# Kernel optimization log

Hardware: AMD Instinct MI355X
Metric: run time of the kernel (lower is better)

Reference implementation:

```python
import jax, jax.numpy as jnp
from jax import lax
import numpy as np

B, N, D_IN = 8, 8192, 16
GROUP_NUM, K = 512, 32
OUT_DIM, N_BLOCKS, DIM_EXP = 256, 2, 2
PREV_DIM = OUT_DIM // DIM_EXP   # 128
MID = OUT_DIM // 2              # bottleneck width in FeatureTransform
C_EXP = 2 * PREV_DIM + 3        # linear1 input channels
EPS = 1e-5                      # BatchNorm eps (eval mode, running stats mean=0 var=1)


def setup_inputs() -> dict:
    ks = jax.random.split(jax.random.key(0), 8)
    return {
        "xyz": jax.random.normal(ks[0], (B, N, 3), jnp.float32),
        "feat": jax.random.normal(ks[1], (B, N, D_IN), jnp.float32),
        "w_embed": jax.random.normal(ks[2], (PREV_DIM, D_IN), jnp.float32) * 0.1,
        "b_embed": jnp.zeros((PREV_DIM,), jnp.float32),
        "g_embed": jnp.ones((PREV_DIM,), jnp.float32),
        "be_embed": jnp.zeros((PREV_DIM,), jnp.float32),
        "w_lin1": jax.random.normal(ks[3], (OUT_DIM, C_EXP), jnp.float32) * 0.05,
        "g_lin1": jnp.ones((OUT_DIM,), jnp.float32),
        "be_lin1": jnp.zeros((OUT_DIM,), jnp.float32),
        "down_w": jax.random.normal(ks[4], (N_BLOCKS, MID, OUT_DIM), jnp.float32) * 0.05,
        "down_b": jnp.zeros((N_BLOCKS, MID), jnp.float32),
        "gd": jnp.ones((N_BLOCKS, MID), jnp.float32),
        "bd": jnp.zeros((N_BLOCKS, MID), jnp.float32),
        "up_w": jax.random.normal(ks[5], (N_BLOCKS, OUT_DIM, MID), jnp.float32) * 0.05,
        "up_b": jnp.zeros((N_BLOCKS, OUT_DIM), jnp.float32),
        "gu": jnp.ones((N_BLOCKS, OUT_DIM), jnp.float32),
        "bu": jnp.zeros((N_BLOCKS, OUT_DIM), jnp.float32),
    }


def _bn(x, g, b, axis):
    # eval-mode BatchNorm with running mean=0, var=1
    shp = [1] * x.ndim
    shp[axis] = -1
    return x / jnp.sqrt(1.0 + EPS) * g.reshape(shp) + b.reshape(shp)


def _fps(xyz, n):
    # deterministic FPS (eval mode): start from point farthest from origin
    Bb, Nn, _ = xyz.shape
    cur0 = jnp.argmax(jnp.sum(xyz * xyz, -1), axis=1)          # [B]
    mind0 = jnp.full((Bb, Nn), 1e10, xyz.dtype)

    def step(carry, _):
        cur, mind = carry
        c = jnp.take_along_axis(xyz, cur[:, None, None], axis=1)  # [B,1,3]
        mind = jnp.minimum(mind, jnp.sum((xyz - c) ** 2, -1))
        return (jnp.argmax(mind, axis=1), mind), cur

    _, sel = lax.scan(step, (cur0, mind0), None, length=n)     # sel: [n,B]
    return sel.T                                               # [B,n]


def _gather(points, idx):
    # points [B,N,C], idx [B,...] -> [B,...,C]
    Bb = points.shape[0]
    flat = idx.reshape(Bb, -1)
    out = jnp.take_along_axis(points, flat[:, :, None], axis=1)
    return out.reshape(idx.shape + (points.shape[-1],))


def _knn(k, ref, query):
    # squared dists, clamped at 0 as in pairwise_sq_dist
    d = (jnp.sum(query * query, -1)[:, :, None]
         + jnp.sum(ref * ref, -1)[:, None, :]
         - 2.0 * jnp.einsum('bsc,bnc->bsn', query, ref))
    d = jnp.maximum(d, 0.0)
    _, idx = lax.top_k(-d, k)
    return idx  # [B,S,k]


def reference(xyz, feat, w_embed, b_embed, g_embed, be_embed, w_lin1, g_lin1, be_lin1,
              down_w, down_b, gd, bd, up_w, up_b, gu, bu):
    # PointEmbed: conv1d(1x1) + BN + ReLU on per-point features -> [B,N,PREV_DIM]
    f0 = jnp.einsum('bnc,dc->bnd', feat, w_embed) + b_embed
    f0 = jax.nn.relu(_bn(f0, g_embed, be_embed, axis=2))

    # FpsKnnGroup
    sel = _fps(xyz, GROUP_NUM)                  # [B,G]
    lc_xyz = _gather(xyz, sel)                  # [B,G,3]
    lc_feat = _gather(f0, sel)                  # [B,G,PREV_DIM]
    nn_idx = _knn(K, xyz, lc_xyz)               # [B,G,K]
    knn_xyz = _gather(xyz, nn_idx)              # [B,G,K,3]
    knn_feat = jnp.concatenate([_gather(f0, nn_idx), knn_xyz], axis=-1)  # [B,G,K,PREV+3]

    # LocalGeoAgg, norm_type='mn40'
    anchor = lc_xyz[:, :, None, :]
    rel_raw = knn_xyz - anchor
    std = jnp.std(rel_raw, ddof=1) + 1e-5       # torch .std() is unbiased
    knn_xyz_n = rel_raw / std
    Bc = knn_feat.shape[0]
    expanded = jnp.concatenate(
        [knn_feat, jnp.broadcast_to(lc_feat[:, :, None, :], (Bc, GROUP_NUM, K, PREV_DIM))],
        axis=-1)                                # [B,G,K,C_EXP]
    x = jnp.einsum('bgkc,dc->bdgk', expanded, w_lin1)   # linear1 (no bias)
    x = jax.nn.relu(_bn(x, g_lin1, be_lin1, axis=1))    # [B,OUT_DIM,G,K]

    # GaussianPosEnc: rel = normalized knn_xyz (perm) minus raw lc_xyz center
    rel = knn_xyz_n.transpose(0, 3, 1, 2) - lc_xyz.transpose(0, 2, 1)[:, :, :, None]
    w = jnp.exp(-jnp.linalg.norm(rel, axis=1) / 2.0)    # sigma=1 -> 2*sigma^2=2
    x = x * w[:, None, :, :]

    # FeatureTransform residual bottlenecks
    for i in range(N_BLOCKS):
        h = jnp.einsum('bcgk,mc->bmgk', x, down_w[i]) + down_b[i][None, :, None, None]
        h = jax.nn.relu(_bn(h, gd[i], bd[i], axis=1))
        h = jnp.einsum('bcgk,mc->bmgk', h, up_w[i]) + up_b[i][None, :, None, None]
        h = _bn(h, gu[i], bu[i], axis=1)
        x = jax.nn.relu(h + x)

    # MaxMeanPool over K
    return jnp.max(x, axis=-1) + jnp.mean(x, axis=-1)   # [B,OUT_DIM,G]
```

## Files before the change

### kernel.cpp

```cpp
#include <hip/hip_runtime.h>

#define B_ 8
#define N_ 8192
#define DIN_ 16
#define G_ 512
#define K_ 32
#define OD_ 256
#define PD_ 128
#define MD_ 128
#define CE_ 259
#define EST 168
#define XST2 264
#define HST 136
#define AL1K 160

typedef __attribute__((ext_vector_type(8))) short short8t;
typedef __attribute__((ext_vector_type(4))) float f32x4;
#define MFMA16(a, b, c) __builtin_amdgcn_mfma_f32_16x16x32_bf16((a), (b), (c), 0, 0, 0)

__device__ __forceinline__ ushort bf16_rne(float x) {
    unsigned u = __float_as_uint(x);
    return (ushort)((u + 0x7FFFu + ((u >> 16) & 1u)) >> 16);
}
__device__ __forceinline__ void bf16_split(float x, ushort& h, ushort& l) {
    h = bf16_rne(x);
    float hf = __uint_as_float((unsigned)h << 16);
    l = bf16_rne(x - hf);
}

#define DPP_STEP_MAXF(x, ctrl) { int _t = __builtin_amdgcn_update_dpp(            \
        __float_as_int(x), __float_as_int(x), (ctrl), 0xF, 0xF, false);           \
        (x) = fmaxf((x), __int_as_float(_t)); }
#define DPP_STEP_MINF(x, ctrl) { int _t = __builtin_amdgcn_update_dpp(            \
        __float_as_int(x), __float_as_int(x), (ctrl), 0xF, 0xF, false);           \
        (x) = fminf((x), __int_as_float(_t)); }
#define DPP_STEP_MINU(x, ctrl) { int _t = __builtin_amdgcn_update_dpp(            \
        (int)(x), (int)(x), (ctrl), 0xF, 0xF, false);                             \
        unsigned _u = (unsigned)_t; (x) = ((x) < _u) ? (x) : _u; }

__device__ __forceinline__ float wave_max_f32(float x) {
    DPP_STEP_MAXF(x, 0x121); DPP_STEP_MAXF(x, 0x122);
    DPP_STEP_MAXF(x, 0x124); DPP_STEP_MAXF(x, 0x128);
    DPP_STEP_MAXF(x, 0x142); DPP_STEP_MAXF(x, 0x143);
    return __int_as_float(__builtin_amdgcn_readlane(__float_as_int(x), 63));
}
__device__ __forceinline__ float wave_min_f32(float x) {
    DPP_STEP_MINF(x, 0x121); DPP_STEP_MINF(x, 0x122);
    DPP_STEP_MINF(x, 0x124); DPP_STEP_MINF(x, 0x128);
    DPP_STEP_MINF(x, 0x142); DPP_STEP_MINF(x, 0x143);
    return __int_as_float(__builtin_amdgcn_readlane(__float_as_int(x), 63));
}
__device__ __forceinline__ unsigned wave_min_u32(unsigned x) {
    DPP_STEP_MINU(x, 0x121); DPP_STEP_MINU(x, 0x122);
    DPP_STEP_MINU(x, 0x124); DPP_STEP_MINU(x, 0x128);
    DPP_STEP_MINU(x, 0x142); DPP_STEP_MINU(x, 0x143);
    return (unsigned)__builtin_amdgcn_readlane((int)x, 63);
}

__global__ __launch_bounds__(256)
void prep_kernel(const float* __restrict__ w_lin1, const float* __restrict__ down_w,
                 const float* __restrict__ up_w, const float* __restrict__ w_embed,
                 float* __restrict__ wta, float* __restrict__ wEtg,
                 ushort* __restrict__ alf, ushort* __restrict__ adf,
                 ushort* __restrict__ auf) {
    int i = blockIdx.x * blockDim.x + threadIdx.x;
    if (i < PD_ * OD_) {
        int j = i >> 8, c = i & 255;
        wta[i] = w_lin1[c * CE_ + 131 + j];
    }
    if (i < DIN_ * PD_) {
        int r = i >> 7, c = i & 127;
        wEtg[i] = w_embed[c * DIN_ + r];
    }
    if (i < 5120) {
        int lane = i & 63, t = i >> 6;
        int kbi = t % 5, mtile = t / 5;
        int m = mtile * 16 + (lane & 15), g16 = lane >> 4;
        int dst = i * 8;
#pragma unroll
        for (int j = 0; j < 8; ++j) {
            int k = kbi * 32 + g16 * 8 + j;
            float v = (k < 131) ? w_lin1[m * CE_ + k] : 0.f;
            ushort h, l; bf16_split(v, h, l);
            alf[dst + j] = h; alf[dst + j + 40960] = l;
        }
    }
    if (i < 8192) {
        int lane = i & 63, t = i >> 6;
        int kbi = t & 7, mtile = (t >> 3) & 7, l = t >> 6;
        int m = mtile * 16 + (lane & 15), g16 = lane >> 4;
        int dst = i * 8;
#pragma unroll
        for (int j = 0; j < 8; ++j) {
            int k = kbi * 32 + g16 * 8 + j;
            float v = down_w[(l * MD_ + m) * OD_ + k];
            ushort h, lo; bf16_split(v, h, lo);
            adf[dst + j] = h; adf[dst + j + 65536] = lo;
        }
    }
    if (i < 8192) {
        int lane = i & 63, t = i >> 6;
        int kbi = t & 3, mtile = (t >> 2) & 15, l = t >> 6;
        int m = mtile * 16 + (lane & 15), g16 = lane >> 4;
        int dst = i * 8;
#pragma unroll
        for (int j = 0; j < 8; ++j) {
            int k = kbi * 32 + g16 * 8 + j;
            float v = up_w[(l * OD_ + m) * MD_ + k];
            ushort h, lo; bf16_split(v, h, lo);
            auf[dst + j] = h; auf[dst + j + 65536] = lo;
        }
    }
}

__global__ __launch_bounds__(512)
void fps_kernel(const float* __restrict__ xyz, int* __restrict__ sel) {
#pragma clang fp contract(off)
    __shared__ float sx[N_], sy[N_], sz[N_];
    __shared__ unsigned long long wred[2][8];
    int b = blockIdx.x, tid = threadIdx.x;
    const float* xb = xyz + (size_t)b * N_ * 3;
    for (int i = tid; i < N_; i += 512) {
        sx[i] = xb[i * 3]; sy[i] = xb[i * 3 + 1]; sz[i] = xb[i * 3 + 2];
    }
    __syncthreads();
    float px[16], py[16], pz[16], mind[16];
#pragma unroll
    for (int j = 0; j < 16; ++j) {
        int idx = tid + j * 512;
        px[j] = sx[idx]; py[j] = sy[idx]; pz[j] = sz[idx];
        mind[j] = 1e10f;
    }
    float tv[16]; int tj[16];
#pragma unroll
    for (int j = 0; j < 16; ++j) {
        tv[j] = (px[j] * px[j] + py[j] * py[j]) + pz[j] * pz[j];
        tj[j] = j;
    }
#pragma unroll
    for (int s = 8; s > 0; s >>= 1)
#pragma unroll
        for (int p = 0; p < 16; p += 16 / s) {
        }
    float v8[8]; int j8[8];
#pragma unroll
    for (int p = 0; p < 8; ++p) { bool t = tv[2*p+1] > tv[2*p]; v8[p] = t ? tv[2*p+1] : tv[2*p]; j8[p] = t ? tj[2*p+1] : tj[2*p]; }
    float v4[4]; int j4[4];
#pragma unroll
    for (int p = 0; p < 4; ++p) { bool t = v8[2*p+1] > v8[2*p]; v4[p] = t ? v8[2*p+1] : v8[2*p]; j4[p] = t ? j8[2*p+1] : j8[2*p]; }
    float v2[2]; int j2[2];
#pragma unroll
    for (int p = 0; p < 2; ++p) { bool t = v4[2*p+1] > v4[2*p]; v2[p] = t ? v4[2*p+1] : v4[2*p]; j2[p] = t ? j4[2*p+1] : j4[2*p]; }
    bool t0 = v2[1] > v2[0];
    float bv = t0 ? v2[1] : v2[0];
    int bi = tid + (t0 ? j2[1] : j2[0]) * 512;

    int wv = tid >> 6;
    {
        float wm = wave_max_f32(bv);
        unsigned mi = (bv == wm) ? (unsigned)bi : 0xFFFFFFFFu;
        unsigned wi = wave_min_u32(mi);
        if ((tid & 63) == 0)
            wred[0][wv] = ((unsigned long long)__float_as_uint(wm) << 32)
                        | (unsigned long long)(0xFFFFFFFFu - wi);
    }
    __syncthreads();
    unsigned long long best = wred[0][0];
#pragma unroll
    for (int i = 1; i < 8; ++i) { unsigned long long v = wred[0][i]; if (v > best) best = v; }
    int cur = (int)(0xFFFFFFFFu - (unsigned)(best & 0xFFFFFFFFull));

    for (int it = 0; it < G_; ++it) {
        if (tid == 0) sel[b * G_ + it] = cur;
        float cx = sx[cur], cy = sy[cur], cz = sz[cur];
#pragma unroll
        for (int j = 0; j < 16; ++j) {
            float dx = px[j] - cx, dy = py[j] - cy, dz = pz[j] - cz;
            float d = (dx * dx + dy * dy) + dz * dz;
            float m = fminf(mind[j], d); mind[j] = m;
        }
#pragma unroll
        for (int p = 0; p < 8; ++p) { bool t = mind[2*p+1] > mind[2*p]; v8[p] = t ? mind[2*p+1] : mind[2*p]; j8[p] = t ? (2*p+1) : (2*p); }
#pragma unroll
        for (int p = 0; p < 4; ++p) { bool t = v8[2*p+1] > v8[2*p]; v4[p] = t ? v8[2*p+1] : v8[2*p]; j4[p] = t ? j8[2*p+1] : j8[2*p]; }
#pragma unroll
        for (int p = 0; p < 2; ++p) { bool t = v4[2*p+1] > v4[2*p]; v2[p] = t ? v4[2*p+1] : v4[2*p]; j2[p] = t ? j4[2*p+1] : j4[2*p]; }
        t0 = v2[1] > v2[0];
        bv = t0 ? v2[1] : v2[0];
        bi = tid + (t0 ? j2[1] : j2[0]) * 512;

        float wm = wave_max_f32(bv);
        unsigned mi = (bv == wm) ? (unsigned)bi : 0xFFFFFFFFu;
        unsigned wi = wave_min_u32(mi);
        int pb = (it + 1) & 1;
        if ((tid & 63) == 0)
            wred[pb][wv] = ((unsigned long long)__float_as_uint(wm) << 32)
                         | (unsigned long long)(0xFFFFFFFFu - wi);
        __syncthreads();
        best = wred[pb][0];
#pragma unroll
        for (int i = 1; i < 8; ++i) { unsigned long long v = wred[pb][i]; if (v > best) best = v; }
        cur = (int)(0xFFFFFFFFu - (unsigned)(best & 0xFFFFFFFFull));
    }
}

__global__ __launch_bounds__(256)
void knn_kernel(const float* __restrict__ xyz, const int* __restrict__ sel,
                int* __restrict__ nn) {
#pragma clang fp contract(off)
    __shared__ float dld[N_];
    __shared__ unsigned long long wred[2][4];
    int gb = blockIdx.x; int b = gb >> 9, s = gb & (G_ - 1);
    const float* xb = xyz + (size_t)b * N_ * 3;
    int q = sel[b * G_ + s];
    float qx = xb[q * 3], qy = xb[q * 3 + 1], qz = xb[q * 3 + 2];
    float qq = (qx * qx + qy * qy) + qz * qz;
    int tid = threadIdx.x;
    const float FINF = __builtin_inff();
    float lv = FINF; int li = tid;
#pragma unroll 4
    for (int j = 0; j < 32; ++j) {
        int n = tid + j * 256;
        float rx = xb[n * 3], ry = xb[n * 3 + 1], rz = xb[n * 3 + 2];
        float rr = (rx * rx + ry * ry) + rz * rz;
        float dt = (qx * rx + qy * ry) + qz * rz;
        float d = (qq + rr) - 2.0f * dt;
        d = fmaxf(d, 0.f);
        dld[n] = d;
        if (d < lv) { lv = d; li = n; }
    }
    {
        float wm = wave_min_f32(lv);
        unsigned mi = (lv == wm) ? (unsigned)li : 0xFFFFFFFFu;
        unsigned wi = wave_min_u32(mi);
        if ((tid & 63) == 0)
            wred[0][tid >> 6] = ((unsigned long long)__float_as_uint(wm) << 32)
                              | (unsigned long long)wi;
    }
    __syncthreads();
    unsigned long long best = wred[0][0];
#pragma unroll
    for (int i = 1; i < 4; ++i) { unsigned long long v = wred[0][i]; if (v < best) best = v; }
    int win = (int)(best & 0xFFFFFFFFull);

    for (int t = 0; t < K_; ++t) {
        if (tid == 0) nn[(size_t)gb * K_ + t] = win;
        if ((win & 255) == tid) {
            dld[win] = FINF;
            lv = FINF; li = tid;
            for (int j = 0; j < 32; ++j) {
                float d = dld[tid + j * 256];
                if (d < lv) { lv = d; li = tid + j * 256; }
            }
        }
        float wm = wave_min_f32(lv);
        unsigned mi = (lv == wm) ? (unsigned)li : 0xFFFFFFFFu;
        unsigned wi = wave_min_u32(mi);
        int pb = (t + 1) & 1;
        if ((tid & 63) == 0)
            wred[pb][tid >> 6] = ((unsigned long long)__float_as_uint(wm) << 32)
                               | (unsigned long long)wi;
        __syncthreads();
        best = wred[pb][0];
#pragma unroll
        for (int i = 1; i < 4; ++i) { unsigned long long v = wred[pb][i]; if (v < best) best = v; }
        win = (int)(best & 0xFFFFFFFFull);
    }
}

__global__ void std_acc_kernel(const float* __restrict__ xyz, const int* __restrict__ sel,
                               const int* __restrict__ nn, double* __restrict__ acc) {
    int tot = B_ * G_ * K_;
    int stride = gridDim.x * blockDim.x;
    double ls = 0.0, lss = 0.0;
    for (int idx = blockIdx.x * blockDim.x + threadIdx.x; idx < tot; idx += stride) {
        int b = idx >> 14; int g = (idx >> 5) & (G_ - 1);
        int n = nn[idx]; int a = sel[b * G_ + g];
        const float* xb = xyz + (size_t)b * N_ * 3;
#pragma unroll
        for (int c = 0; c < 3; ++c) {
            float v = xb[n * 3 + c] - xb[a * 3 + c];
            ls += (double)v; lss += (double)v * (double)v;
        }
    }
#pragma unroll
    for (int off = 32; off > 0; off >>= 1) {
        ls += __shfl_down(ls, off); lss += __shfl_down(lss, off);
    }
    if ((threadIdx.x & 63) == 0) { atomicAdd(acc, ls); atomicAdd(acc + 1, lss); }
}

__global__ void std_fin_kernel(const double* __restrict__ acc, float* __restrict__ stdp) {
    double s = acc[0], ss = acc[1];
    double M = (double)(B_ * G_ * K_ * 3);
    double var = (ss - s * s / M) / (M - 1.0);
    stdp[0] = (float)sqrt(var) + 1e-5f;
}

__global__ __launch_bounds__(256, 3)
void group_kernel(const float* __restrict__ xyz, const float* __restrict__ feat,
                  const float* __restrict__ wEtg, const float* __restrict__ bE,
                  const float* __restrict__ gE, const float* __restrict__ beE,
                  const int* __restrict__ sel, const int* __restrict__ nn,
                  const float* __restrict__ wta,
                  const ushort* __restrict__ alf, const ushort* __restrict__ adf,
                  const ushort* __restrict__ auf,
                  const float* __restrict__ g_lin1, const float* __restrict__ be_lin1,
                  const float* __restrict__ down_b, const float* __restrict__ gd,
                  const float* __restrict__ bd,
                  const float* __restrict__ up_b, const float* __restrict__ gu,
                  const float* __restrict__ bu,
                  const float* __restrict__ stdp, float* __restrict__ out) {
    __shared__ __align__(16) ushort smem[25600];
    __shared__ float lcv_s[OD_];
    __shared__ float wk_s[K_];
    __shared__ int nns_s[K_];
    __shared__ float anch[3];
    ushort* XTh = smem;
    ushort* XTl = smem + 8448;
    ushort* HTh = smem + 16896;
    ushort* HTl = smem + 21248;
    ushort* Ehi = XTh;
    ushort* Elo = XTl;
    float* wEt = (float*)(smem + 16896);
    float* fL  = wEt + 2048;
    float* lcf = fL + 544;

    int gb = blockIdx.x; int b = gb >> 9, g = gb & (G_ - 1);
    int tid = threadIdx.x;
    const float* xb = xyz + (size_t)b * N_ * 3;
    int a = sel[b * G_ + g];
    if (tid < K_) nns_s[tid] = nn[(size_t)gb * K_ + tid];
    if (tid < 3)  anch[tid] = xb[a * 3 + tid];
    __syncthreads();

    for (int idx = tid; idx < DIN_ * PD_; idx += 256) wEt[idx] = wEtg[idx];
    const float* fb = feat + (size_t)b * N_ * DIN_;
    for (int idx = tid; idx < 33 * DIN_; idx += 256) {
        int k = idx >> 4, j = idx & 15;
        int n = (k < K_) ? nns_s[k] : a;
        fL[idx] = fb[(size_t)n * DIN_ + j];
    }
    __syncthreads();

    const float s_bn = 1.0f / sqrtf(1.0f + 1e-5f);
    for (int idx = tid; idx < 33 * PD_; idx += 256) {
        int k = idx >> 7, c = idx & 127;
        const float* f = &fL[k * DIN_];
        float acc2 = 0.f;
#pragma unroll
        for (int i = 0; i < DIN_; ++i) acc2 += wEt[i * PD_ + c] * f[i];
        acc2 = (acc2 + bE[c]) * s_bn * gE[c] + beE[c];
        acc2 = fmaxf(acc2, 0.f);
        if (k < K_) { ushort h, l; bf16_split(acc2, h, l); Ehi[k * EST + c] = h; Elo[k * EST + c] = l; }
        else lcf[c] = acc2;
    }
    for (int idx = tid; idx < K_ * 32; idx += 256) {
        int k = idx >> 5, c = 128 + (idx & 31);
        ushort h = 0, l = 0;
        if (c < 131) { float v = xb[nns_s[k] * 3 + (c - 128)]; bf16_split(v, h, l); }
        Ehi[k * EST + c] = h; Elo[k * EST + c] = l;
    }
    if (tid < K_) {
#pragma clang fp contract(off)
        float sd = stdp[0];
        int n = nns_s[tid];
        float rx = (xb[n * 3]     - anch[0]) / sd - anch[0];
        float ry = (xb[n * 3 + 1] - anch[1]) / sd - anch[1];
        float rz = (xb[n * 3 + 2] - anch[2]) / sd - anch[2];
        float nrm = sqrtf((rx * rx + ry * ry) + rz * rz);
        wk_s[tid] = expf(-0.5f * nrm);
    }
    __syncthreads();
    {
        float s = 0.f;
        for (int j = 0; j < PD_; ++j) s += wta[j * OD_ + tid] * lcf[j];
        lcv_s[tid] = s;
    }
    __syncthreads();

    int wv = tid >> 6, lane = tid & 63;
    int g16 = lane >> 4, r16 = lane & 15;
    int lane8 = lane * 8;

    f32x4 accl[4][2];
#pragma unroll
    for (int mt = 0; mt < 4; ++mt) {
        int mc = 64 * wv + 16 * mt + 4 * g16;
        float4 lv = *(const float4*)&lcv_s[mc];
        f32x4 iv = {lv.x, lv.y, lv.z, lv.w};
        accl[mt][0] = iv; accl[mt][1] = iv;
    }
    {
        int eb0 = r16 * EST + g16 * 8;
        int eb1 = (r16 + 16) * EST + g16 * 8;
        for (int kbi = 0; kbi < 5; ++kbi) {
            int kb = kbi * 32;
            short8t eh0 = *(const short8t*)&Ehi[eb0 + kb];
            short8t el0 = *(const short8t*)&Elo[eb0 + kb];
            short8t eh1 = *(const short8t*)&Ehi[eb1 + kb];
            short8t el1 = *(const short8t*)&Elo[eb1 + kb];
#pragma unroll
            for (int mt = 0; mt < 4; ++mt) {
                const ushort* wp = alf + (((4 * wv + mt) * 5 + kbi) << 9) + lane8;
                short8t wh = *(const short8t*)wp;
                short8t wl = *(const short8t*)(wp + 40960);
                accl[mt][0] = MFMA16(wh, eh0, accl[mt][0]);
                accl[mt][1] = MFMA16(wh, eh1, accl[mt][1]);
                accl[mt][0] = MFMA16(wh, el0, accl[mt][0]);
                accl[mt][1] = MFMA16(wh, el1, accl[mt][1]);
                accl[mt][0] = MFMA16(wl, eh0, accl[mt][0]);
                accl[mt][1] = MFMA16(wl, eh1, accl[mt][1]);
            }
        }
    }
    __syncthreads();
    {
        float w0 = wk_s[r16], w1 = wk_s[r16 + 16];
#pragma unroll
        for (int mt = 0; mt < 4; ++mt) {
            int mc = 64 * wv + 16 * mt + 4 * g16;
            float4 gg = *(const float4*)&g_lin1[mc];
            float4 bb = *(const float4*)&be_lin1[mc];
            float ga[4] = {gg.x, gg.y, gg.z, gg.w};
            float ba[4] = {bb.x, bb.y, bb.z, bb.w};
            ushort h0[4], l0[4], h1[4], l1[4];
#pragma unroll
            for (int r = 0; r < 4; ++r) {
                float v0 = fmaxf(accl[mt][0][r] * s_bn * ga[r] + ba[r], 0.f) * w0;
                float v1 = fmaxf(accl[mt][1][r] * s_bn * ga[r] + ba[r], 0.f) * w1;
                bf16_split(v0, h0[r], l0[r]);
                bf16_split(v1, h1[r], l1[r]);
            }
            *(ushort4*)&XTh[r16 * XST2 + mc] = make_ushort4(h0[0], h0[1], h0[2], h0[3]);
            *(ushort4*)&XTl[r16 * XST2 + mc] = make_ushort4(l0[0], l0[1], l0[2], l0[3]);
            *(ushort4*)&XTh[(r16 + 16) * XST2 + mc] = make_ushort4(h1[0], h1[1], h1[2], h1[3]);
            *(ushort4*)&XTl[(r16 + 16) * XST2 + mc] = make_ushort4(l1[0], l1[1], l1[2], l1[3]);
        }
    }
    __syncthreads();

    int xbo0 = r16 * XST2 + g16 * 8;
    int xbo1 = (r16 + 16) * XST2 + g16 * 8;
    int hbo0 = r16 * HST + g16 * 8;
    int hbo1 = (r16 + 16) * HST + g16 * 8;
    const f32x4 zz = {0.f, 0.f, 0.f, 0.f};
    const float inv_k = 1.0f / 32.0f;

    for (int l = 0; l < 2; ++l) {
        f32x4 accd[2][2];
        accd[0][0] = zz; accd[0][1] = zz; accd[1][0] = zz; accd[1][1] = zz;
        for (int kbi = 0; kbi < 8; ++kbi) {
            int kb = kbi * 32;
            short8t xh0 = *(const short8t*)&XTh[xbo0 + kb];
            short8t xl0 = *(const short8t*)&XTl[xbo0 + kb];
            short8t xh1 = *(const short8t*)&XTh[xbo1 + kb];
            short8t xl1 = *(const short8t*)&XTl[xbo1 + kb];
#pragma unroll
            for (int mt = 0; mt < 2; ++mt) {
                const ushort* wp = adf + (((l * 8 + (2 * wv + mt)) * 8 + kbi) << 9) + lane8;
                short8t wh = *(const short8t*)wp;
                short8t wl = *(const short8t*)(wp + 65536);
                accd[mt][0] = MFMA16(wh, xh0, accd[mt][0]);
                accd[mt][1] = MFMA16(wh, xh1, accd[mt][1]);
                accd[mt][0] = MFMA16(wh, xl0, accd[mt][0]);
                accd[mt][1] = MFMA16(wh, xl1, accd[mt][1]);
                accd[mt][0] = MFMA16(wl, xh0, accd[mt][0]);
                accd[mt][1] = MFMA16(wl, xh1, accd[mt][1]);
            }
        }
#pragma unroll
        for (int mt = 0; mt < 2; ++mt) {
            int mc = 32 * wv + 16 * mt + 4 * g16;
            float4 db = *(const float4*)&down_b[l * MD_ + mc];
            float4 gv = *(const float4*)&gd[l * MD_ + mc];
            float4 bv = *(const float4*)&bd[l * MD_ + mc];
            float dba[4] = {db.x, db.y, db.z, db.w};
            float gva[4] = {gv.x, gv.y, gv.z, gv.w};
            float bva[4] = {bv.x, bv.y, bv.z, bv.w};
            ushort h0[4], l0[4], h1[4], l1[4];
#pragma unroll
            for (int r = 0; r < 4; ++r) {
                float v0 = fmaxf((accd[mt][0][r] + dba[r]) * s_bn * gva[r] + bva[r], 0.f);
                float v1 = fmaxf((accd[mt][1][r] + dba[r]) * s_bn * gva[r] + bva[r], 0.f);
                bf16_split(v0, h0[r], l0[r]);
                bf16_split(v1, h1[r], l1[r]);
            }
            *(ushort4*)&HTh[r16 * HST + mc] = make_ushort4(h0[0], h0[1], h0[2], h0[3]);
            *(ushort4*)&HTl[r16 * HST + mc] = make_ushort4(l0[0], l0[1], l0[2], l0[3]);
            *(ushort4*)&HTh[(r16 + 16) * HST + mc] = make_ushort4(h1[0], h1[1], h1[2], h1[3]);
            *(ushort4*)&HTl[(r16 + 16) * HST + mc] = make_ushort4(l1[0], l1[1], l1[2], l1[3]);
        }
        __syncthreads();

        f32x4 accu[4][2];
#pragma unroll
        for (int mt = 0; mt < 4; ++mt) { accu[mt][0] = zz; accu[mt][1] = zz; }
        for (int kbi = 0; kbi < 4; ++kbi) {
            int kb = kbi * 32;
            short8t hh0 = *(const short8t*)&HTh[hbo0 + kb];
            short8t hl0 = *(const short8t*)&HTl[hbo0 + kb];
            short8t hh1 = *(const short8t*)&HTh[hbo1 + kb];
            short8t hl1 = *(const short8t*)&HTl[hbo1 + kb];
#pragma unroll
            for (int mt = 0; mt < 4; ++mt) {
                const ushort* wp = auf + (((l * 16 + (4 * wv + mt)) * 4 + kbi) << 9) + lane8;
                short8t wh = *(const short8t*)wp;
                short8t wl = *(const short8t*)(wp + 65536);
                accu[mt][0] = MFMA16(wh, hh0, accu[mt][0]);
                accu[mt][1] = MFMA16(wh, hh1, accu[mt][1]);
                accu[mt][0] = MFMA16(wh, hl0, accu[mt][0]);
                accu[mt][1] = MFMA16(wh, hl1, accu[mt][1]);
                accu[mt][0] = MFMA16(wl, hh0, accu[mt][0]);
                accu[mt][1] = MFMA16(wl, hh1, accu[mt][1]);
            }
        }
#pragma unroll
        for (int mt = 0; mt < 4; ++mt) {
            int mc = 64 * wv + 16 * mt + 4 * g16;
            float4 ub = *(const float4*)&up_b[l * OD_ + mc];
            float4 gv = *(const float4*)&gu[l * OD_ + mc];
            float4 bv = *(const float4*)&bu[l * OD_ + mc];
            float uba[4] = {ub.x, ub.y, ub.z, ub.w};
            float gva[4] = {gv.x, gv.y, gv.z, gv.w};
            float bva[4] = {bv.x, bv.y, bv.z, bv.w};
            ushort4 xh0 = *(const ushort4*)&XTh[r16 * XST2 + mc];
            ushort4 xl0 = *(const ushort4*)&XTl[r16 * XST2 + mc];
            ushort4 xh1 = *(const ushort4*)&XTh[(r16 + 16) * XST2 + mc];
            ushort4 xl1 = *(const ushort4*)&XTl[(r16 + 16) * XST2 + mc];
            ushort xha0[4] = {xh0.x, xh0.y, xh0.z, xh0.w};
            ushort xla0[4] = {xl0.x, xl0.y, xl0.z, xl0.w};
            ushort xha1[4] = {xh1.x, xh1.y, xh1.z, xh1.w};
            ushort xla1[4] = {xl1.x, xl1.y, xl1.z, xl1.w};
            float nx0[4], nx1[4];
#pragma unroll
            for (int r = 0; r < 4; ++r) {
                float xf0 = __uint_as_float((unsigned)xha0[r] << 16) + __uint_as_float((unsigned)xla0[r] << 16);
                float xf1 = __uint_as_float((unsigned)xha1[r] << 16) + __uint_as_float((unsigned)xla1[r] << 16);
                float v0 = (accu[mt][0][r] + uba[r]) * s_bn * gva[r] + bva[r];
                float v1 = (accu[mt][1][r] + uba[r]) * s_bn * gva[r] + bva[r];
                nx0[r] = fmaxf(v0 + xf0, 0.f);
                nx1[r] = fmaxf(v1 + xf1, 0.f);
            }
            if (l == 0) {
                ushort h0[4], l0[4], h1[4], l1[4];
#pragma unroll
                for (int r = 0; r < 4; ++r) {
                    bf16_split(nx0[r], h0[r], l0[r]);
                    bf16_split(nx1[r], h1[r], l1[r]);
                }
                *(ushort4*)&XTh[r16 * XST2 + mc] = make_ushort4(h0[0], h0[1], h0[2], h0[3]);
                *(ushort4*)&XTl[r16 * XST2 + mc] = make_ushort4(l0[0], l0[1], l0[2], l0[3]);
                *(ushort4*)&XTh[(r16 + 16) * XST2 + mc] = make_ushort4(h1[0], h1[1], h1[2], h1[3]);
                *(ushort4*)&XTl[(r16 + 16) * XST2 + mc] = make_ushort4(l1[0], l1[1], l1[2], l1[3]);
            } else {
#pragma unroll
                for (int r = 0; r < 4; ++r) {
                    float mx = fmaxf(nx0[r], nx1[r]);
                    float sm = nx0[r] + nx1[r];
#pragma unroll
                    for (int off = 1; off < 16; off <<= 1) {
                        mx = fmaxf(mx, __shfl_xor(mx, off));
                        sm += __shfl_xor(sm, off);
                    }
                    if (r16 == 0)
                        out[((size_t)(b * OD_ + mc + r)) * G_ + g] = mx + sm * inv_k;
                }
            }
        }
        __syncthreads();
    }
}

extern "C" void kernel_launch(void* const* d_in, const int* in_sizes, int n_in,
                              void* d_out, int out_size, void* d_ws, size_t ws_size,
                              hipStream_t stream) {
    const float* xyz     = (const float*)d_in[0];
    const float* feat    = (const float*)d_in[1];
    const float* w_embed = (const float*)d_in[2];
    const float* b_embed = (const float*)d_in[3];
    const float* g_embed = (const float*)d_in[4];
    const float* be_embed= (const float*)d_in[5];
    const float* w_lin1  = (const float*)d_in[6];
    const float* g_lin1  = (const float*)d_in[7];
    const float* be_lin1 = (const float*)d_in[8];
    const float* down_w  = (const float*)d_in[9];
    const float* down_b  = (const float*)d_in[10];
    const float* gd      = (const float*)d_in[11];
    const float* bd      = (const float*)d_in[12];
    const float* up_w    = (const float*)d_in[13];
    const float* up_b    = (const float*)d_in[14];
    const float* gu      = (const float*)d_in[15];
    const float* bu      = (const float*)d_in[16];
    float* out = (float*)d_out;

    char* w = (char*)d_ws;
    float* wta   = (float*)w;  w += PD_ * OD_ * 4;
    float* wEtg  = (float*)w;  w += DIN_ * PD_ * 4;
    ushort* alf  = (ushort*)w; w += 2 * 40960 * 2;
    ushort* adf  = (ushort*)w; w += 2 * 65536 * 2;
    ushort* auf  = (ushort*)w; w += 2 * 65536 * 2;
    int* sel     = (int*)w;    w += B_ * G_ * 4;
    int* nn      = (int*)w;    w += B_ * G_ * K_ * 4;
    double* acc  = (double*)w; w += 16;
    float* stdp  = (float*)w;

    hipMemsetAsync(acc, 0, 2 * sizeof(double), stream);
    prep_kernel<<<256, 256, 0, stream>>>(w_lin1, down_w, up_w, w_embed,
                                         wta, wEtg, alf, adf, auf);
    fps_kernel<<<B_, 512, 0, stream>>>(xyz, sel);
    knn_kernel<<<B_ * G_, 256, 0, stream>>>(xyz, sel, nn);
    std_acc_kernel<<<256, 256, 0, stream>>>(xyz, sel, nn, acc);
    std_fin_kernel<<<1, 1, 0, stream>>>(acc, stdp);
    group_kernel<<<B_ * G_, 256, 0, stream>>>(xyz, feat, wEtg, b_embed, g_embed, be_embed,
        sel, nn, wta, alf, adf, auf, g_lin1, be_lin1, down_b, gd, bd, up_b, gu, bu, stdp, out);
}
```

Before: 1.091 ms.

## Carry winner coordinates through FPS reduction, drop LDS point copy, vectorize embed

FPS no longer stages all points in LDS. Each thread keeps a running argmax inside the distance loop and publishes the winning point's coordinates through shared memory alongside the index, which removes the tree reduction and the per-iteration LDS lookup of the centroid. Selected indices in FPS and kNN are buffered in shared memory and written out once at the end. The embedding MLP now computes four channels per thread with float4 loads and packed stores. The in-loop strict-greater argmax keeps the lowest index on ties, but the wpt write relies on exactly one lane matching the wave winner.

```diff
diff --git a/kernel.cpp b/kernel.cpp
--- a/kernel.cpp
+++ b/kernel.cpp
@@ -116,45 +116,21 @@
 __global__ __launch_bounds__(512)
 void fps_kernel(const float* __restrict__ xyz, int* __restrict__ sel) {
 #pragma clang fp contract(off)
-    __shared__ float sx[N_], sy[N_], sz[N_];
     __shared__ unsigned long long wred[2][8];
+    __shared__ float4 wpt[2][8];
+    __shared__ int sel_s[G_];
     int b = blockIdx.x, tid = threadIdx.x;
     const float* xb = xyz + (size_t)b * N_ * 3;
-    for (int i = tid; i < N_; i += 512) {
-        sx[i] = xb[i * 3]; sy[i] = xb[i * 3 + 1]; sz[i] = xb[i * 3 + 2];
-    }
-    __syncthreads();
     float px[16], py[16], pz[16], mind[16];
+    float bv = -1.f, bx = 0.f, by = 0.f, bz = 0.f; int bi = 0;
 #pragma unroll
     for (int j = 0; j < 16; ++j) {
         int idx = tid + j * 512;
-        px[j] = sx[idx]; py[j] = sy[idx]; pz[j] = sz[idx];
+        px[j] = xb[idx * 3]; py[j] = xb[idx * 3 + 1]; pz[j] = xb[idx * 3 + 2];
         mind[j] = 1e10f;
-    }
-    float tv[16]; int tj[16];
-#pragma unroll
-    for (int j = 0; j < 16; ++j) {
-        tv[j] = (px[j] * px[j] + py[j] * py[j]) + pz[j] * pz[j];
-        tj[j] = j;
-    }
-#pragma unroll
-    for (int s = 8; s > 0; s >>= 1)
-#pragma unroll
-        for (int p = 0; p < 16; p += 16 / s) {
-        }
-    float v8[8]; int j8[8];
-#pragma unroll
-    for (int p = 0; p < 8; ++p) { bool t = tv[2*p+1] > tv[2*p]; v8[p] = t ? tv[2*p+1] : tv[2*p]; j8[p] = t ? tj[2*p+1] : tj[2*p]; }
-    float v4[4]; int j4[4];
-#pragma unroll
-    for (int p = 0; p < 4; ++p) { bool t = v8[2*p+1] > v8[2*p]; v4[p] = t ? v8[2*p+1] : v8[2*p]; j4[p] = t ? j8[2*p+1] : j8[2*p]; }
-    float v2[2]; int j2[2];
-#pragma unroll
-    for (int p = 0; p < 2; ++p) { bool t = v4[2*p+1] > v4[2*p]; v2[p] = t ? v4[2*p+1] : v4[2*p]; j2[p] = t ? j4[2*p+1] : j4[2*p]; }
-    bool t0 = v2[1] > v2[0];
-    float bv = t0 ? v2[1] : v2[0];
-    int bi = tid + (t0 ? j2[1] : j2[0]) * 512;
-
+        float ss = (px[j] * px[j] + py[j] * py[j]) + pz[j] * pz[j];
+        if (ss > bv) { bv = ss; bi = idx; bx = px[j]; by = py[j]; bz = pz[j]; }
+    }
     int wv = tid >> 6;
     {
         float wm = wave_max_f32(bv);
@@ -163,32 +139,27 @@
         if ((tid & 63) == 0)
             wred[0][wv] = ((unsigned long long)__float_as_uint(wm) << 32)
                         | (unsigned long long)(0xFFFFFFFFu - wi);
-    }
-    __syncthreads();
-    unsigned long long best = wred[0][0];
-#pragma unroll
-    for (int i = 1; i < 8; ++i) { unsigned long long v = wred[0][i]; if (v > best) best = v; }
+        if (bv == wm && (unsigned)bi == wi)
+            wpt[0][wv] = make_float4(bx, by, bz, 0.f);
+    }
+    __syncthreads();
+    unsigned long long best = wred[0][0]; int wb = 0;
+#pragma unroll
+    for (int i = 1; i < 8; ++i) { unsigned long long v = wred[0][i]; if (v > best) { best = v; wb = i; } }
     int cur = (int)(0xFFFFFFFFu - (unsigned)(best & 0xFFFFFFFFull));
+    float4 cc = wpt[0][wb];
+    float cx = cc.x, cy = cc.y, cz = cc.z;
 
     for (int it = 0; it < G_; ++it) {
-        if (tid == 0) sel[b * G_ + it] = cur;
-        float cx = sx[cur], cy = sy[cur], cz = sz[cur];
+        if (tid == 0) sel_s[it] = cur;
+        bv = -1.f; bi = 0; bx = 0.f; by = 0.f; bz = 0.f;
 #pragma unroll
         for (int j = 0; j < 16; ++j) {
             float dx = px[j] - cx, dy = py[j] - cy, dz = pz[j] - cz;
             float d = (dx * dx + dy * dy) + dz * dz;
             float m = fminf(mind[j], d); mind[j] = m;
-        }
-#pragma unroll
-        for (int p = 0; p < 8; ++p) { bool t = mind[2*p+1] > mind[2*p]; v8[p] = t ? mind[2*p+1] : mind[2*p]; j8[p] = t ? (2*p+1) : (2*p); }
-#pragma unroll
-        for (int p = 0; p < 4; ++p) { bool t = v8[2*p+1] > v8[2*p]; v4[p] = t ? v8[2*p+1] : v8[2*p]; j4[p] = t ? j8[2*p+1] : j8[2*p]; }
-#pragma unroll
-        for (int p = 0; p < 2; ++p) { bool t = v4[2*p+1] > v4[2*p]; v2[p] = t ? v4[2*p+1] : v4[2*p]; j2[p] = t ? j4[2*p+1] : j4[2*p]; }
-        t0 = v2[1] > v2[0];
-        bv = t0 ? v2[1] : v2[0];
-        bi = tid + (t0 ? j2[1] : j2[0]) * 512;
-
+            if (m > bv) { bv = m; bi = tid + j * 512; bx = px[j]; by = py[j]; bz = pz[j]; }
+        }
         float wm = wave_max_f32(bv);
         unsigned mi = (bv == wm) ? (unsigned)bi : 0xFFFFFFFFu;
         unsigned wi = wave_min_u32(mi);
@@ -196,12 +167,18 @@
         if ((tid & 63) == 0)
             wred[pb][wv] = ((unsigned long long)__float_as_uint(wm) << 32)
                          | (unsigned long long)(0xFFFFFFFFu - wi);
+        if (bv == wm && (unsigned)bi == wi)
+            wpt[pb][wv] = make_float4(bx, by, bz, 0.f);
         __syncthreads();
-        best = wred[pb][0];
-#pragma unroll
-        for (int i = 1; i < 8; ++i) { unsigned long long v = wred[pb][i]; if (v > best) best = v; }
+        best = wred[pb][0]; wb = 0;
+#pragma unroll
+        for (int i = 1; i < 8; ++i) { unsigned long long v = wred[pb][i]; if (v > best) { best = v; wb = i; } }
         cur = (int)(0xFFFFFFFFu - (unsigned)(best & 0xFFFFFFFFull));
-    }
+        cc = wpt[pb][wb];
+        cx = cc.x; cy = cc.y; cz = cc.z;
+    }
+    __syncthreads();
+    sel[b * G_ + tid] = sel_s[tid];
 }
 
 __global__ __launch_bounds__(256)
@@ -210,6 +187,7 @@
 #pragma clang fp contract(off)
     __shared__ float dld[N_];
     __shared__ unsigned long long wred[2][4];
+    __shared__ int nn_s[K_];
     int gb = blockIdx.x; int b = gb >> 9, s = gb & (G_ - 1);
     const float* xb = xyz + (size_t)b * N_ * 3;
     int q = sel[b * G_ + s];
@@ -244,7 +222,7 @@
     int win = (int)(best & 0xFFFFFFFFull);
 
     for (int t = 0; t < K_; ++t) {
-        if (tid == 0) nn[(size_t)gb * K_ + t] = win;
+        if (tid == 0) nn_s[t] = win;
         if ((win & 255) == tid) {
             dld[win] = FINF;
             lv = FINF; li = tid;
@@ -266,6 +244,7 @@
         for (int i = 1; i < 4; ++i) { unsigned long long v = wred[pb][i]; if (v < best) best = v; }
         win = (int)(best & 0xFFFFFFFFull);
     }
+    if (tid < K_) nn[(size_t)gb * K_ + tid] = nn_s[tid];
 }
 
 __global__ void std_acc_kernel(const float* __restrict__ xyz, const int* __restrict__ sel,
@@ -344,16 +323,32 @@
     __syncthreads();
 
     const float s_bn = 1.0f / sqrtf(1.0f + 1e-5f);
-    for (int idx = tid; idx < 33 * PD_; idx += 256) {
-        int k = idx >> 7, c = idx & 127;
+    for (int t = tid; t < 33 * 32; t += 256) {
+        int k = t >> 5, c0 = (t & 31) * 4;
         const float* f = &fL[k * DIN_];
-        float acc2 = 0.f;
-#pragma unroll
-        for (int i = 0; i < DIN_; ++i) acc2 += wEt[i * PD_ + c] * f[i];
-        acc2 = (acc2 + bE[c]) * s_bn * gE[c] + beE[c];
-        acc2 = fmaxf(acc2, 0.f);
-        if (k < K_) { ushort h, l; bf16_split(acc2, h, l); Ehi[k * EST + c] = h; Elo[k * EST + c] = l; }
-        else lcf[c] = acc2;
+        float a0 = 0.f, a1 = 0.f, a2 = 0.f, a3 = 0.f;
+#pragma unroll
+        for (int i = 0; i < DIN_; ++i) {
+            float4 w4 = *(const float4*)&wEt[i * PD_ + c0];
+            float fv = f[i];
+            a0 += w4.x * fv; a1 += w4.y * fv; a2 += w4.z * fv; a3 += w4.w * fv;
+        }
+        float4 b4  = *(const float4*)&bE[c0];
+        float4 g4  = *(const float4*)&gE[c0];
+        float4 be4 = *(const float4*)&beE[c0];
+        float o0 = fmaxf((a0 + b4.x) * s_bn * g4.x + be4.x, 0.f);
+        float o1 = fmaxf((a1 + b4.y) * s_bn * g4.y + be4.y, 0.f);
+        float o2 = fmaxf((a2 + b4.z) * s_bn * g4.z + be4.z, 0.f);
+        float o3 = fmaxf((a3 + b4.w) * s_bn * g4.w + be4.w, 0.f);
+        if (k < K_) {
+            ushort h0, l0, h1, l1, h2, l2, h3, l3;
+            bf16_split(o0, h0, l0); bf16_split(o1, h1, l1);
+            bf16_split(o2, h2, l2); bf16_split(o3, h3, l3);
+            *(ushort4*)&Ehi[k * EST + c0] = make_ushort4(h0, h1, h2, h3);
+            *(ushort4*)&Elo[k * EST + c0] = make_ushort4(l0, l1, l2, l3);
+        } else {
+            *(float4*)&lcf[c0] = make_float4(o0, o1, o2, o3);
+        }
     }
     for (int idx = tid; idx < K_ * 32; idx += 256) {
         int k = idx >> 5, c = 128 + (idx & 31);
```

After: 1.102 ms. About the same (+1.0%).
